# Performance work log

Measured on AMD Instinct MI355X. Metric: run time of the kernel, lower is better.

## Reference

```python
import jax, jax.numpy as jnp
import numpy as np

BETA = 5.0
B, D, K, E2 = 64, 3072, 512, 64


def setup_inputs() -> dict:
    key = jax.random.key(0)
    k1, k2, k3, k4 = jax.random.split(key, 4)
    images = jax.random.normal(k1, (B, D), dtype=jnp.float32)
    w_proj = jax.random.normal(k2, (K, D), dtype=jnp.float32) * 0.02   # project.weight
    w_img2 = jax.random.normal(k3, (K, D * E2), dtype=jnp.float32) * 0.02  # img2.weight
    w_rec = jax.random.normal(k4, (E2, K), dtype=jnp.float32) * 0.02   # rec.weight
    return {"images": images, "w_proj": w_proj, "w_img2": w_img2, "w_rec": w_rec}


def reference(images, w_proj, w_img2, w_rec):
    beta = BETA
    wimg = w_proj.T            # (D, K)
    wrec = w_rec.T             # (K, E2)
    # img2.weight (K, D*E2) -> codebook tensor (K, D, E2), std-normalized over D (ddof=1 to match torch)
    wimg2 = w_img2.reshape(K, D, E2)
    wimg2 = wimg2 / (0.01 + jnp.std(wimg2, axis=1, keepdims=True, ddof=1))

    # ---- encode ----
    xd = images[:, :, None] - wimg[None]          # (B, D, K)
    xh = -jnp.mean(xd * xd, axis=1) * beta        # (B, K)
    xp = jax.nn.softmax(xh, axis=-1)              # (B, K)
    lat1 = xp @ wrec                              # (B, E2)
    xe = jnp.einsum('bdk,kde->bke', xd, wimg2)    # (B, K, E2)
    lat2 = jnp.einsum('bke,bk->be', xe, xp)       # (B, E2)

    # ---- decode ----
    diff = lat1[:, :, None] - wrec.T[None]        # (B, E2, K); wrec.T is (E2, K)
    xh2 = -jnp.mean(diff * diff, axis=1) * beta   # (B, K)
    xp2 = jax.nn.softmax(xh2, axis=-1)            # (B, K)
    xx = xp2[:, :, None] * lat2[:, None, :]       # (B, K, E2)
    xd2 = jnp.einsum('bke,kde->bd', xx, wimg2)    # (B, D)
    images_recon = xp2 @ wimg.T + xd2             # (B, D)

    loss = jnp.mean((images_recon - images) ** 2, axis=-1)  # (B,)
    return loss
```

## Files before the change

kernel.cpp:

```cpp
#include <hip/hip_runtime.h>
#include <math.h>

#define Bn 64
#define Dn 3072
#define Kn 512
#define En 64

static constexpr float BETA = 5.0f;

static constexpr size_t ZF_OFF    = 0;
static constexpr size_t ACCP_OFF  = 1048576;
static constexpr size_t PART_OFF  = 1048576;
static constexpr size_t STATP_OFF = 5242880;
static constexpr size_t S_OFF     = 5439488;
static constexpr size_t PACC_OFF  = 5472256;
static constexpr size_t DOTP_OFF  = 5505024;
static constexpr size_t NPP_OFF   = 5767168;
static constexpr size_t XP2_OFF   = 5771264;
static constexpr size_t XP2B_OFF  = 5804032;
static constexpr size_t LAT2_OFF  = 5820416;
static constexpr size_t WRECT_OFF = 5824512;
static constexpr size_t FRAG_OFF  = 5857280;

typedef float  f4  __attribute__((ext_vector_type(4)));
typedef __bf16 bf8 __attribute__((ext_vector_type(8)));
typedef int    i4  __attribute__((ext_vector_type(4)));

union AB { i4 i; bf8 b; };

__device__ __forceinline__ unsigned short bf16b(float x) {
  __bf16 h = (__bf16)x;
  union Cv { __bf16 h; unsigned short u; } c;
  c.h = h;
  return c.u;
}

__device__ __forceinline__ float waveAllMax(float v) {
#pragma unroll
  for (int o = 32; o; o >>= 1) v = fmaxf(v, __shfl_xor(v, o));
  return v;
}
__device__ __forceinline__ float waveAllSum(float v) {
#pragma unroll
  for (int o = 32; o; o >>= 1) v += __shfl_xor(v, o);
  return v;
}

__global__ __launch_bounds__(256) void kPT(const float* __restrict__ img,
                                           const float* __restrict__ wrec,
                                           float* __restrict__ ws) {
  const int t = threadIdx.x;
  if (blockIdx.x < 96) {
    const int ds = blockIdx.x;
    const int T = t >> 6, l = t & 63;
    const int b = 16 * T + (l & 15);
    const int d0 = 32 * ds + 8 * (l >> 4);
    const float* p = img + (size_t)b * Dn + d0;
    unsigned short u[8];
#pragma unroll
    for (int j = 0; j < 8; ++j) u[j] = bf16b(p[j]);
    i4 v;
    v.x = (int)u[0] | ((int)u[1] << 16);
    v.y = (int)u[2] | ((int)u[3] << 16);
    v.z = (int)u[4] | ((int)u[5] << 16);
    v.w = (int)u[6] | ((int)u[7] << 16);
    ((i4*)(ws + FRAG_OFF))[(ds * 4 + T) * 64 + l] = v;
  } else {
    int g = (blockIdx.x - 96) * 256 + t;
    int k = g >> 6, e = g & 63;
    ws[WRECT_OFF + g] = wrec[(size_t)e * Kn + k];
  }
}

__global__ __launch_bounds__(256) void kDotP(const float* __restrict__ wproj,
                                             float* __restrict__ ws) {
  const int t = threadIdx.x, w = t >> 6, l = t & 63, elane = l & 15, dgrp = l >> 4;
  const int kk = blockIdx.x * 16 + elane;
  const int dc = blockIdx.y;
  const int n0 = dc * 12;
  const i4* afr = (const i4*)(ws + FRAG_OFF);
  const float* wrow = wproj + (size_t)kk * Dn;
  f4 acc = {0.f, 0.f, 0.f, 0.f};
  float np = 0.f;
  float bwA[8], bwB[8];
  i4 avA, avB;
  avA = afr[((size_t)n0 * 4 + w) * 64 + l];
#pragma unroll
  for (int j = 0; j < 8; ++j) bwA[j] = wrow[(size_t)n0 * 32 + 8 * dgrp + j];

#define KD_ITER(BWC, BWN, AVC, AVN, NL) {                                        \
    const int nl1 = (NL) + 1;                                                    \
    if (nl1 < 12) {                                                              \
      AVN = afr[((size_t)(n0 + nl1) * 4 + w) * 64 + l];                          \
      _Pragma("unroll")                                                          \
      for (int j = 0; j < 8; ++j)                                                \
        BWN[j] = wrow[(size_t)(n0 + nl1) * 32 + 8 * dgrp + j];                   \
    }                                                                            \
    bf8 bfr;                                                                     \
    _Pragma("unroll")                                                            \
    for (int j = 0; j < 8; ++j) { float v = BWC[j]; np = fmaf(v, v, np); bfr[j] = (__bf16)v; } \
    AB a; a.i = AVC;                                                             \
    acc = __builtin_amdgcn_mfma_f32_16x16x32_bf16(a.b, bfr, acc, 0, 0, 0);       \
  }

  for (int nl = 0; nl < 12; nl += 2) {
    KD_ITER(bwA, bwB, avA, avB, nl)
    KD_ITER(bwB, bwA, avB, avA, nl + 1)
  }
#undef KD_ITER
#pragma unroll
  for (int r = 0; r < 4; ++r) {
    int b = 16 * w + 4 * dgrp + r;
    ws[DOTP_OFF + (size_t)dc * (Bn * Kn) + (size_t)b * Kn + kk] = acc[r];
  }
  np += __shfl_xor(np, 16);
  np += __shfl_xor(np, 32);
  if (w == 0 && dgrp == 0) ws[NPP_OFF + (size_t)dc * Kn + kk] = np;
}

__global__ __launch_bounds__(256, 4) void kA(const float* __restrict__ wproj,
                                             const float* __restrict__ w2,
                                             float* __restrict__ ws) {
  const int k = blockIdx.x, h = blockIdx.y, t = threadIdx.x;
  const int w = t >> 6, l = t & 63, elane = l & 15, dgrp = l >> 4;
  const int ecol = 16 * w + elane;
  const int n0 = h * 48;
  __shared__ float wp[Dn / 2];
  const float* wpk = wproj + (size_t)k * Dn + (size_t)h * (Dn / 2);
  {
    f4* dst = (f4*)wp;
    const f4* src = (const f4*)wpk;
    dst[t] = src[t];
    if (t < 128) dst[t + 256] = src[t + 256];
  }
  __syncthreads();

  const i4* afr = (const i4*)(ws + FRAG_OFF);
  const float* w2k = w2 + (size_t)k * (Dn * En);
  f4 acc0 = {0.f,0.f,0.f,0.f}, acc1 = {0.f,0.f,0.f,0.f};
  f4 acc2 = {0.f,0.f,0.f,0.f}, acc3 = {0.f,0.f,0.f,0.f};
  float ssum = 0.f, ssq = 0.f, pacc = 0.f;
  float bwA[8], bwB[8];
#pragma unroll
  for (int j = 0; j < 8; ++j)
    bwA[j] = w2k[(size_t)(n0 * 32 + 8 * dgrp + j) * 64 + ecol];

#define KA_ITER(BWC, BWN, NL) {                                                  \
    const int nl1 = (NL) + 1;                                                    \
    if (nl1 < 48) {                                                              \
      _Pragma("unroll")                                                          \
      for (int j = 0; j < 8; ++j)                                                \
        BWN[j] = w2k[(size_t)((n0 + nl1) * 32 + 8 * dgrp + j) * 64 + ecol];      \
    }                                                                            \
    i4 av0 = afr[((size_t)(n0 + (NL)) * 4 + 0) * 64 + l];                        \
    i4 av1 = afr[((size_t)(n0 + (NL)) * 4 + 1) * 64 + l];                        \
    i4 av2 = afr[((size_t)(n0 + (NL)) * 4 + 2) * 64 + l];                        \
    i4 av3 = afr[((size_t)(n0 + (NL)) * 4 + 3) * 64 + l];                        \
    bf8 bfr;                                                                     \
    _Pragma("unroll")                                                            \
    for (int j = 0; j < 8; ++j) {                                                \
      float v = BWC[j];                                                          \
      ssum += v; ssq = fmaf(v, v, ssq);                                          \
      pacc = fmaf(wp[(NL) * 32 + 8 * dgrp + j], v, pacc);                        \
      bfr[j] = (__bf16)v;                                                        \
    }                                                                            \
    AB a0, a1, a2, a3;                                                           \
    a0.i = av0; a1.i = av1; a2.i = av2; a3.i = av3;                              \
    acc0 = __builtin_amdgcn_mfma_f32_16x16x32_bf16(a0.b, bfr, acc0, 0, 0, 0);    \
    acc1 = __builtin_amdgcn_mfma_f32_16x16x32_bf16(a1.b, bfr, acc1, 0, 0, 0);    \
    acc2 = __builtin_amdgcn_mfma_f32_16x16x32_bf16(a2.b, bfr, acc2, 0, 0, 0);    \
    acc3 = __builtin_amdgcn_mfma_f32_16x16x32_bf16(a3.b, bfr, acc3, 0, 0, 0);    \
  }

  for (int nl = 0; nl < 48; nl += 2) {
    KA_ITER(bwA, bwB, nl)
    KA_ITER(bwB, bwA, nl + 1)
  }
#undef KA_ITER

  ssum += __shfl_xor(ssum, 16); ssum += __shfl_xor(ssum, 32);
  ssq  += __shfl_xor(ssq, 16);  ssq  += __shfl_xor(ssq, 32);
  pacc += __shfl_xor(pacc, 16); pacc += __shfl_xor(pacc, 32);
  const size_t kh = (size_t)(k * 2 + h);
  if (dgrp == 0) {
    ws[STATP_OFF + kh * 192 + 0 * 64 + ecol] = ssum;
    ws[STATP_OFF + kh * 192 + 1 * 64 + ecol] = ssq;
    ws[STATP_OFF + kh * 192 + 2 * 64 + ecol] = pacc;
  }
#pragma unroll
  for (int T = 0; T < 4; ++T) {
    f4 a = (T == 0) ? acc0 : (T == 1) ? acc1 : (T == 2) ? acc2 : acc3;
#pragma unroll
    for (int r = 0; r < 4; ++r) {
      int b = 16 * T + 4 * dgrp + r;
      ws[ACCP_OFF + kh * 4096 + (size_t)b * 64 + ecol] = a[r];
    }
  }
}

__global__ __launch_bounds__(64) void kStat(float* __restrict__ ws) {
  const int k = blockIdx.x, e = threadIdx.x;
  const size_t o0 = STATP_OFF + (size_t)(2 * k) * 192;
  const size_t o1 = STATP_OFF + (size_t)(2 * k + 1) * 192;
  float ssum = ws[o0 + e] + ws[o1 + e];
  float ssq  = ws[o0 + 64 + e] + ws[o1 + 64 + e];
  float pacc = ws[o0 + 128 + e] + ws[o1 + 128 + e];
  float var = (ssq - ssum * ssum * (1.0f / Dn)) * (1.0f / (Dn - 1));
  float sv = 1.0f / (0.01f + sqrtf(fmaxf(var, 0.f)));
  ws[S_OFF + (size_t)k * 64 + e] = sv;
  ws[PACC_OFF + (size_t)k * 64 + e] = pacc;
}

__global__ __launch_bounds__(256) void kMid(const float* __restrict__ img,
                                            float* __restrict__ ws) {
  const int b = blockIdx.x;
  const int t = threadIdx.x;
  const int wid = t >> 6, lane = t & 63;
  __shared__ float xp_sh[512];
  __shared__ float red[16];
  __shared__ float scratch[256];
  __shared__ __align__(16) float l1_sh[64];

  float acc = 0.f;
  const f4* irow = (const f4*)(img + (size_t)b * Dn);
#pragma unroll
  for (int i = 0; i < 3; ++i) {
    f4 v = irow[t + 256 * i];
    acc = fmaf(v.x, v.x, acc); acc = fmaf(v.y, v.y, acc);
    acc = fmaf(v.z, v.z, acc); acc = fmaf(v.w, v.w, acc);
  }
  acc = waveAllSum(acc);
  if (lane == 0) red[wid] = acc;
  __syncthreads();
  const float nimg = red[0] + red[1] + red[2] + red[3];

  float d1 = 0.f, d2 = 0.f, npa = 0.f, npb = 0.f;
#pragma unroll
  for (int dc = 0; dc < 8; ++dc) {
    d1  += ws[DOTP_OFF + (size_t)dc * (Bn * Kn) + (size_t)b * Kn + t];
    d2  += ws[DOTP_OFF + (size_t)dc * (Bn * Kn) + (size_t)b * Kn + t + 256];
    npa += ws[NPP_OFF + (size_t)dc * Kn + t];
    npb += ws[NPP_OFF + (size_t)dc * Kn + t + 256];
  }
  const float c = -(BETA / Dn);
  float x1 = c * (nimg - 2.f * d1 + npa);
  float x2 = c * (nimg - 2.f * d2 + npb);

  float m = waveAllMax(fmaxf(x1, x2));
  if (lane == 0) red[4 + wid] = m;
  __syncthreads();
  m = fmaxf(fmaxf(red[4], red[5]), fmaxf(red[6], red[7]));
  float e1 = expf(x1 - m), e2 = expf(x2 - m);
  float sv = waveAllSum(e1 + e2);
  if (lane == 0) red[8 + wid] = sv;
  __syncthreads();
  float inv = 1.f / (red[8] + red[9] + red[10] + red[11]);
  xp_sh[t] = e1 * inv;
  xp_sh[t + 256] = e2 * inv;
  __syncthreads();

  const int e = t & 63, q = t >> 6;
  float lacc = 0.f;
  for (int kk = q * 128; kk < q * 128 + 128; ++kk)
    lacc = fmaf(xp_sh[kk], ws[WRECT_OFF + (size_t)kk * En + e], lacc);
  scratch[q * 64 + e] = lacc;
  __syncthreads();
  if (t < 64)
    l1_sh[t] = scratch[t] + scratch[64 + t] + scratch[128 + t] + scratch[192 + t];
  __syncthreads();

  float l2acc = 0.f;
  for (int kk = q * 128; kk < q * 128 + 128; ++kk) {
    float a = ws[ACCP_OFF + (size_t)(2 * kk) * 4096 + (size_t)b * 64 + e]
            + ws[ACCP_OFF + (size_t)(2 * kk + 1) * 4096 + (size_t)b * 64 + e];
    l2acc = fmaf(xp_sh[kk] * ws[S_OFF + (size_t)kk * 64 + e],
                 a - ws[PACC_OFF + (size_t)kk * 64 + e], l2acc);
  }
  __syncthreads();
  scratch[q * 64 + e] = l2acc;
  __syncthreads();
  if (t < 64)
    ws[LAT2_OFF + (size_t)b * En + t] =
        scratch[t] + scratch[64 + t] + scratch[128 + t] + scratch[192 + t];

  float h1 = 0.f, h2 = 0.f;
#pragma unroll
  for (int i = 0; i < 16; ++i) {
    f4 lv = *(const f4*)&l1_sh[i * 4];
    f4 w1 = *(const f4*)&ws[WRECT_OFF + (size_t)t * En + i * 4];
    f4 w2v = *(const f4*)&ws[WRECT_OFF + ((size_t)t + 256) * En + i * 4];
    float a0 = lv.x - w1.x, a1 = lv.y - w1.y, a2 = lv.z - w1.z, a3 = lv.w - w1.w;
    h1 = fmaf(a0, a0, h1); h1 = fmaf(a1, a1, h1);
    h1 = fmaf(a2, a2, h1); h1 = fmaf(a3, a3, h1);
    float b0 = lv.x - w2v.x, b1 = lv.y - w2v.y, b2 = lv.z - w2v.z, b3 = lv.w - w2v.w;
    h2 = fmaf(b0, b0, h2); h2 = fmaf(b1, b1, h2);
    h2 = fmaf(b2, b2, h2); h2 = fmaf(b3, b3, h2);
  }
  const float c2 = -(BETA / En);
  x1 = c2 * h1; x2 = c2 * h2;

  m = waveAllMax(fmaxf(x1, x2));
  if (lane == 0) red[4 + wid] = m;
  __syncthreads();
  m = fmaxf(fmaxf(red[4], red[5]), fmaxf(red[6], red[7]));
  e1 = expf(x1 - m); e2 = expf(x2 - m);
  sv = waveAllSum(e1 + e2);
  if (lane == 0) red[8 + wid] = sv;
  __syncthreads();
  inv = 1.f / (red[8] + red[9] + red[10] + red[11]);
  float p1 = e1 * inv, p2 = e2 * inv;
  ws[XP2_OFF + (size_t)b * Kn + t] = p1;
  ws[XP2_OFF + (size_t)b * Kn + t + 256] = p2;
  unsigned short* xpb = (unsigned short*)(ws + XP2B_OFF);
  xpb[(size_t)b * Kn + t] = bf16b(p1);
  xpb[(size_t)b * Kn + t + 256] = bf16b(p2);
}

__global__ __launch_bounds__(256) void kZ(float* __restrict__ ws) {
  const int g = blockIdx.x * 256 + threadIdx.x;
  const int S = g >> 8;
  const int T = (g >> 6) & 3;
  const int l = g & 63;
  const int dgrp = l >> 4;
  const int b = 16 * T + (l & 15);
  const int kd0 = S * 32 + 8 * dgrp;
  const int k = kd0 >> 6;
  const int e0 = kd0 & 63;
  const float xp2v = ws[XP2_OFF + (size_t)b * Kn + k];
  unsigned short u[8];
#pragma unroll
  for (int j = 0; j < 8; ++j) {
    float v = xp2v * ws[LAT2_OFF + (size_t)b * En + e0 + j] * ws[S_OFF + (size_t)k * En + e0 + j];
    u[j] = bf16b(v);
  }
  i4 v;
  v.x = (int)u[0] | ((int)u[1] << 16);
  v.y = (int)u[2] | ((int)u[3] << 16);
  v.z = (int)u[4] | ((int)u[5] << 16);
  v.w = (int)u[6] | ((int)u[7] << 16);
  ((i4*)(ws + ZF_OFF))[g] = v;
}

__global__ __launch_bounds__(256, 3) void kB(const float* __restrict__ wproj,
                                             const float* __restrict__ w2,
                                             float* __restrict__ ws) {
  const int dtile = blockIdx.x, ks = blockIdx.y, t = threadIdx.x;
  const int w = t >> 6, l = t & 63, elane = l & 15, dgrp = l >> 4;
  const int d = dtile * 64 + 16 * w + elane;
  const i4* zfr = (const i4*)(ws + ZF_OFF);
  f4 acc0 = {0.f,0.f,0.f,0.f}, acc1 = {0.f,0.f,0.f,0.f};
  f4 acc2 = {0.f,0.f,0.f,0.f}, acc3 = {0.f,0.f,0.f,0.f};
  f4 bwA[2], bwB[2];
  i4 avA[4], avB[4];
  {
    const f4* p = (const f4*)(w2 + ((size_t)(ks * 32) * Dn + d) * En + 8 * dgrp);
    bwA[0] = p[0]; bwA[1] = p[1];
#pragma unroll
    for (int T = 0; T < 4; ++T) avA[T] = zfr[((size_t)(ks * 64) * 4 + T) * 64 + l];
  }

#define KB_ITER(BWC, BWN, AVC, AVN, N) {                                         \
    const int np1 = (N) + 1;                                                     \
    if (np1 < 64) {                                                              \
      const int kk = ks * 32 + (np1 >> 1);                                       \
      const int e0 = (np1 & 1) * 32;                                             \
      const f4* p = (const f4*)(w2 + ((size_t)kk * Dn + d) * En + e0 + 8 * dgrp);\
      BWN[0] = p[0]; BWN[1] = p[1];                                              \
      _Pragma("unroll")                                                          \
      for (int T = 0; T < 4; ++T)                                                \
        AVN[T] = zfr[((size_t)(ks * 64 + np1) * 4 + T) * 64 + l];                \
    }                                                                            \
    bf8 bfr;                                                                     \
    _Pragma("unroll")                                                            \
    for (int j = 0; j < 4; ++j) {                                                \
      bfr[j] = (__bf16)BWC[0][j];                                                \
      bfr[4 + j] = (__bf16)BWC[1][j];                                            \
    }                                                                            \
    AB a0, a1, a2, a3;                                                           \
    a0.i = AVC[0]; a1.i = AVC[1]; a2.i = AVC[2]; a3.i = AVC[3];                  \
    acc0 = __builtin_amdgcn_mfma_f32_16x16x32_bf16(a0.b, bfr, acc0, 0, 0, 0);    \
    acc1 = __builtin_amdgcn_mfma_f32_16x16x32_bf16(a1.b, bfr, acc1, 0, 0, 0);    \
    acc2 = __builtin_amdgcn_mfma_f32_16x16x32_bf16(a2.b, bfr, acc2, 0, 0, 0);    \
    acc3 = __builtin_amdgcn_mfma_f32_16x16x32_bf16(a3.b, bfr, acc3, 0, 0, 0);    \
  }

  for (int n = 0; n < 64; n += 2) {
    KB_ITER(bwA, bwB, avA, avB, n)
    KB_ITER(bwB, bwA, avB, avA, n + 1)
  }
#undef KB_ITER

  {
    const int kk0 = ks * 32;
    bf8 bw;
#pragma unroll
    for (int j = 0; j < 8; ++j)
      bw[j] = (__bf16)wproj[(size_t)(kk0 + 8 * dgrp + j) * Dn + d];
    const unsigned short* xpb = (const unsigned short*)(ws + XP2B_OFF);
    AB a0, a1, a2, a3;
    a0.i = *(const i4*)&xpb[(size_t)(0 * 16 + elane) * Kn + kk0 + 8 * dgrp];
    a1.i = *(const i4*)&xpb[(size_t)(1 * 16 + elane) * Kn + kk0 + 8 * dgrp];
    a2.i = *(const i4*)&xpb[(size_t)(2 * 16 + elane) * Kn + kk0 + 8 * dgrp];
    a3.i = *(const i4*)&xpb[(size_t)(3 * 16 + elane) * Kn + kk0 + 8 * dgrp];
    acc0 = __builtin_amdgcn_mfma_f32_16x16x32_bf16(a0.b, bw, acc0, 0, 0, 0);
    acc1 = __builtin_amdgcn_mfma_f32_16x16x32_bf16(a1.b, bw, acc1, 0, 0, 0);
    acc2 = __builtin_amdgcn_mfma_f32_16x16x32_bf16(a2.b, bw, acc2, 0, 0, 0);
    acc3 = __builtin_amdgcn_mfma_f32_16x16x32_bf16(a3.b, bw, acc3, 0, 0, 0);
  }

#pragma unroll
  for (int T = 0; T < 4; ++T) {
    f4 a = (T == 0) ? acc0 : (T == 1) ? acc1 : (T == 2) ? acc2 : acc3;
#pragma unroll
    for (int r = 0; r < 4; ++r) {
      int b = 16 * T + 4 * dgrp + r;
      ws[PART_OFF + ((size_t)ks * Bn + b) * Dn + d] = a[r];
    }
  }
}

__global__ __launch_bounds__(256) void kLoss(const float* __restrict__ img,
                                             const float* __restrict__ ws,
                                             float* __restrict__ out) {
  const int b = blockIdx.x, t = threadIdx.x;
  __shared__ float red[4];
  float acc = 0.f;
  const f4* p4 = (const f4*)(ws + PART_OFF);
  const f4* i4p = (const f4*)(img + (size_t)b * Dn);
  const int rowq = Dn / 4;
#pragma unroll
  for (int i = 0; i < 3; ++i) {
    int idx = t + 256 * i;
    f4 r = {0.f, 0.f, 0.f, 0.f};
#pragma unroll
    for (int s = 0; s < 16; ++s)
      r += p4[((size_t)s * Bn + b) * rowq + idx];
    f4 v = i4p[idx];
    float dx = r.x - v.x, dy = r.y - v.y, dz = r.z - v.z, dw = r.w - v.w;
    acc = fmaf(dx, dx, acc); acc = fmaf(dy, dy, acc);
    acc = fmaf(dz, dz, acc); acc = fmaf(dw, dw, acc);
  }
  acc = waveAllSum(acc);
  if ((t & 63) == 0) red[t >> 6] = acc;
  __syncthreads();
  if (t == 0) out[b] = (red[0] + red[1] + red[2] + red[3]) * (1.0f / Dn);
}

extern "C" void kernel_launch(void* const* d_in, const int* in_sizes, int n_in,
                              void* d_out, int out_size, void* d_ws, size_t ws_size,
                              hipStream_t stream) {
  const float* img   = (const float*)d_in[0];
  const float* wproj = (const float*)d_in[1];
  const float* w2    = (const float*)d_in[2];
  const float* wrec  = (const float*)d_in[3];
  float* ws  = (float*)d_ws;
  float* out = (float*)d_out;

  hipLaunchKernelGGL(kPT,   dim3(224), dim3(256), 0, stream, img, wrec, ws);
  hipLaunchKernelGGL(kDotP, dim3(32, 8), dim3(256), 0, stream, wproj, ws);
  hipLaunchKernelGGL(kA,    dim3(512, 2), dim3(256), 0, stream, wproj, w2, ws);
  hipLaunchKernelGGL(kStat, dim3(512), dim3(64), 0, stream, ws);
  hipLaunchKernelGGL(kMid,  dim3(64),  dim3(256), 0, stream, img, ws);
  hipLaunchKernelGGL(kZ,    dim3(1024), dim3(256), 0, stream, ws);
  hipLaunchKernelGGL(kB,    dim3(48, 16), dim3(256), 0, stream, wproj, w2, ws);
  hipLaunchKernelGGL(kLoss, dim3(64),  dim3(256), 0, stream, img, ws, out);
}
```

Measured before the change: 254.6 us.

## Fuse image-projection dot products into kA and z-fragment build into kMid

```diff
diff --git a/kernel.cpp b/kernel.cpp
--- a/kernel.cpp
+++ b/kernel.cpp
@@ -15,12 +15,10 @@
 static constexpr size_t S_OFF     = 5439488;
 static constexpr size_t PACC_OFF  = 5472256;
 static constexpr size_t DOTP_OFF  = 5505024;
-static constexpr size_t NPP_OFF   = 5767168;
-static constexpr size_t XP2_OFF   = 5771264;
-static constexpr size_t XP2B_OFF  = 5804032;
-static constexpr size_t LAT2_OFF  = 5820416;
-static constexpr size_t WRECT_OFF = 5824512;
-static constexpr size_t FRAG_OFF  = 5857280;
+static constexpr size_t NPROJ_OFF = 5570560;
+static constexpr size_t XP2B_OFF  = 5571072;
+static constexpr size_t WRECT_OFF = 5587456;
+static constexpr size_t FRAG_OFF  = 5620224;
 
 typedef float  f4  __attribute__((ext_vector_type(4)));
 typedef __bf16 bf8 __attribute__((ext_vector_type(8)));
@@ -72,52 +70,6 @@
   }
 }
 
-__global__ __launch_bounds__(256) void kDotP(const float* __restrict__ wproj,
-                                             float* __restrict__ ws) {
-  const int t = threadIdx.x, w = t >> 6, l = t & 63, elane = l & 15, dgrp = l >> 4;
-  const int kk = blockIdx.x * 16 + elane;
-  const int dc = blockIdx.y;
-  const int n0 = dc * 12;
-  const i4* afr = (const i4*)(ws + FRAG_OFF);
-  const float* wrow = wproj + (size_t)kk * Dn;
-  f4 acc = {0.f, 0.f, 0.f, 0.f};
-  float np = 0.f;
-  float bwA[8], bwB[8];
-  i4 avA, avB;
-  avA = afr[((size_t)n0 * 4 + w) * 64 + l];
-#pragma unroll
-  for (int j = 0; j < 8; ++j) bwA[j] = wrow[(size_t)n0 * 32 + 8 * dgrp + j];
-
-#define KD_ITER(BWC, BWN, AVC, AVN, NL) {                                        \
-    const int nl1 = (NL) + 1;                                                    \
-    if (nl1 < 12) {                                                              \
-      AVN = afr[((size_t)(n0 + nl1) * 4 + w) * 64 + l];                          \
-      _Pragma("unroll")                                                          \
-      for (int j = 0; j < 8; ++j)                                                \
-        BWN[j] = wrow[(size_t)(n0 + nl1) * 32 + 8 * dgrp + j];                   \
-    }                                                                            \
-    bf8 bfr;                                                                     \
-    _Pragma("unroll")                                                            \
-    for (int j = 0; j < 8; ++j) { float v = BWC[j]; np = fmaf(v, v, np); bfr[j] = (__bf16)v; } \
-    AB a; a.i = AVC;                                                             \
-    acc = __builtin_amdgcn_mfma_f32_16x16x32_bf16(a.b, bfr, acc, 0, 0, 0);       \
-  }
-
-  for (int nl = 0; nl < 12; nl += 2) {
-    KD_ITER(bwA, bwB, avA, avB, nl)
-    KD_ITER(bwB, bwA, avB, avA, nl + 1)
-  }
-#undef KD_ITER
-#pragma unroll
-  for (int r = 0; r < 4; ++r) {
-    int b = 16 * w + 4 * dgrp + r;
-    ws[DOTP_OFF + (size_t)dc * (Bn * Kn) + (size_t)b * Kn + kk] = acc[r];
-  }
-  np += __shfl_xor(np, 16);
-  np += __shfl_xor(np, 32);
-  if (w == 0 && dgrp == 0) ws[NPP_OFF + (size_t)dc * Kn + kk] = np;
-}
-
 __global__ __launch_bounds__(256, 4) void kA(const float* __restrict__ wproj,
                                              const float* __restrict__ w2,
                                              float* __restrict__ ws) {
@@ -126,12 +78,19 @@
   const int ecol = 16 * w + elane;
   const int n0 = h * 48;
   __shared__ float wp[Dn / 2];
+  __shared__ __bf16 wpb[Dn / 2];
   const float* wpk = wproj + (size_t)k * Dn + (size_t)h * (Dn / 2);
-  {
-    f4* dst = (f4*)wp;
-    const f4* src = (const f4*)wpk;
-    dst[t] = src[t];
-    if (t < 128) dst[t + 256] = src[t + 256];
+  if (t < 192) {
+    f4 x = ((const f4*)wpk)[2 * t];
+    f4 y = ((const f4*)wpk)[2 * t + 1];
+    ((f4*)wp)[2 * t] = x;
+    ((f4*)wp)[2 * t + 1] = y;
+    i4 v;
+    v.x = (int)bf16b(x.x) | ((int)bf16b(x.y) << 16);
+    v.y = (int)bf16b(x.z) | ((int)bf16b(x.w) << 16);
+    v.z = (int)bf16b(y.x) | ((int)bf16b(y.y) << 16);
+    v.w = (int)bf16b(y.z) | ((int)bf16b(y.w) << 16);
+    ((i4*)wpb)[t] = v;
   }
   __syncthreads();
 
@@ -139,23 +98,27 @@
   const float* w2k = w2 + (size_t)k * (Dn * En);
   f4 acc0 = {0.f,0.f,0.f,0.f}, acc1 = {0.f,0.f,0.f,0.f};
   f4 acc2 = {0.f,0.f,0.f,0.f}, acc3 = {0.f,0.f,0.f,0.f};
+  f4 dac0 = {0.f,0.f,0.f,0.f}, dac1 = {0.f,0.f,0.f,0.f};
+  f4 dac2 = {0.f,0.f,0.f,0.f}, dac3 = {0.f,0.f,0.f,0.f};
   float ssum = 0.f, ssq = 0.f, pacc = 0.f;
   float bwA[8], bwB[8];
+  i4 avA[4], avB[4];
 #pragma unroll
   for (int j = 0; j < 8; ++j)
     bwA[j] = w2k[(size_t)(n0 * 32 + 8 * dgrp + j) * 64 + ecol];
-
-#define KA_ITER(BWC, BWN, NL) {                                                  \
+#pragma unroll
+  for (int T = 0; T < 4; ++T) avA[T] = afr[((size_t)n0 * 4 + T) * 64 + l];
+
+#define KA_STEP(BWC, BWN, AVC, AVN, NL) {                                        \
     const int nl1 = (NL) + 1;                                                    \
     if (nl1 < 48) {                                                              \
       _Pragma("unroll")                                                          \
       for (int j = 0; j < 8; ++j)                                                \
         BWN[j] = w2k[(size_t)((n0 + nl1) * 32 + 8 * dgrp + j) * 64 + ecol];      \
+      _Pragma("unroll")                                                          \
+      for (int T = 0; T < 4; ++T)                                                \
+        AVN[T] = afr[((size_t)(n0 + nl1) * 4 + T) * 64 + l];                     \
     }                                                                            \
-    i4 av0 = afr[((size_t)(n0 + (NL)) * 4 + 0) * 64 + l];                        \
-    i4 av1 = afr[((size_t)(n0 + (NL)) * 4 + 1) * 64 + l];                        \
-    i4 av2 = afr[((size_t)(n0 + (NL)) * 4 + 2) * 64 + l];                        \
-    i4 av3 = afr[((size_t)(n0 + (NL)) * 4 + 3) * 64 + l];                        \
     bf8 bfr;                                                                     \
     _Pragma("unroll")                                                            \
     for (int j = 0; j < 8; ++j) {                                                \
@@ -164,19 +127,24 @@
       pacc = fmaf(wp[(NL) * 32 + 8 * dgrp + j], v, pacc);                        \
       bfr[j] = (__bf16)v;                                                        \
     }                                                                            \
+    bf8 wfr = *(const bf8*)&wpb[(NL) * 32 + 8 * dgrp];                           \
     AB a0, a1, a2, a3;                                                           \
-    a0.i = av0; a1.i = av1; a2.i = av2; a3.i = av3;                              \
+    a0.i = AVC[0]; a1.i = AVC[1]; a2.i = AVC[2]; a3.i = AVC[3];                  \
     acc0 = __builtin_amdgcn_mfma_f32_16x16x32_bf16(a0.b, bfr, acc0, 0, 0, 0);    \
     acc1 = __builtin_amdgcn_mfma_f32_16x16x32_bf16(a1.b, bfr, acc1, 0, 0, 0);    \
     acc2 = __builtin_amdgcn_mfma_f32_16x16x32_bf16(a2.b, bfr, acc2, 0, 0, 0);    \
     acc3 = __builtin_amdgcn_mfma_f32_16x16x32_bf16(a3.b, bfr, acc3, 0, 0, 0);    \
+    dac0 = __builtin_amdgcn_mfma_f32_16x16x32_bf16(a0.b, wfr, dac0, 0, 0, 0);    \
+    dac1 = __builtin_amdgcn_mfma_f32_16x16x32_bf16(a1.b, wfr, dac1, 0, 0, 0);    \
+    dac2 = __builtin_amdgcn_mfma_f32_16x16x32_bf16(a2.b, wfr, dac2, 0, 0, 0);    \
+    dac3 = __builtin_amdgcn_mfma_f32_16x16x32_bf16(a3.b, wfr, dac3, 0, 0, 0);    \
   }
 
   for (int nl = 0; nl < 48; nl += 2) {
-    KA_ITER(bwA, bwB, nl)
-    KA_ITER(bwB, bwA, nl + 1)
-  }
-#undef KA_ITER
+    KA_STEP(bwA, bwB, avA, avB, nl)
+    KA_STEP(bwB, bwA, avB, avA, nl + 1)
+  }
+#undef KA_STEP
 
   ssum += __shfl_xor(ssum, 16); ssum += __shfl_xor(ssum, 32);
   ssq  += __shfl_xor(ssq, 16);  ssq  += __shfl_xor(ssq, 32);
@@ -187,6 +155,17 @@
     ws[STATP_OFF + kh * 192 + 1 * 64 + ecol] = ssq;
     ws[STATP_OFF + kh * 192 + 2 * 64 + ecol] = pacc;
   }
+  if (w == 0 && elane == 0) {
+#pragma unroll
+    for (int T = 0; T < 4; ++T) {
+      f4 d = (T == 0) ? dac0 : (T == 1) ? dac1 : (T == 2) ? dac2 : dac3;
+#pragma unroll
+      for (int r = 0; r < 4; ++r) {
+        int b = 16 * T + 4 * dgrp + r;
+        ws[DOTP_OFF + (size_t)h * (Bn * Kn) + (size_t)b * Kn + k] = d[r];
+      }
+    }
+  }
 #pragma unroll
   for (int T = 0; T < 4; ++T) {
     f4 a = (T == 0) ? acc0 : (T == 1) ? acc1 : (T == 2) ? acc2 : acc3;
@@ -198,7 +177,8 @@
   }
 }
 
-__global__ __launch_bounds__(64) void kStat(float* __restrict__ ws) {
+__global__ __launch_bounds__(64) void kStat(const float* __restrict__ wproj,
+                                            float* __restrict__ ws) {
   const int k = blockIdx.x, e = threadIdx.x;
   const size_t o0 = STATP_OFF + (size_t)(2 * k) * 192;
   const size_t o1 = STATP_OFF + (size_t)(2 * k + 1) * 192;
@@ -209,6 +189,15 @@
   float sv = 1.0f / (0.01f + sqrtf(fmaxf(var, 0.f)));
   ws[S_OFF + (size_t)k * 64 + e] = sv;
   ws[PACC_OFF + (size_t)k * 64 + e] = pacc;
+  float np = 0.f;
+  const float* wr = wproj + (size_t)k * Dn;
+#pragma unroll 8
+  for (int i = 0; i < 48; ++i) {
+    float v = wr[i * 64 + e];
+    np = fmaf(v, v, np);
+  }
+  np = waveAllSum(np);
+  if (e == 0) ws[NPROJ_OFF + k] = np;
 }
 
 __global__ __launch_bounds__(256) void kMid(const float* __restrict__ img,
@@ -218,8 +207,9 @@
   const int wid = t >> 6, lane = t & 63;
   __shared__ float xp_sh[512];
   __shared__ float red[16];
-  __shared__ float scratch[256];
+  __shared__ __align__(16) float scratch[1024];
   __shared__ __align__(16) float l1_sh[64];
+  __shared__ float l2_sh[64];
 
   float acc = 0.f;
   const f4* irow = (const f4*)(img + (size_t)b * Dn);
@@ -234,17 +224,15 @@
   __syncthreads();
   const float nimg = red[0] + red[1] + red[2] + red[3];
 
-  float d1 = 0.f, d2 = 0.f, npa = 0.f, npb = 0.f;
-#pragma unroll
-  for (int dc = 0; dc < 8; ++dc) {
-    d1  += ws[DOTP_OFF + (size_t)dc * (Bn * Kn) + (size_t)b * Kn + t];
-    d2  += ws[DOTP_OFF + (size_t)dc * (Bn * Kn) + (size_t)b * Kn + t + 256];
-    npa += ws[NPP_OFF + (size_t)dc * Kn + t];
-    npb += ws[NPP_OFF + (size_t)dc * Kn + t + 256];
-  }
+  float d1 = ws[DOTP_OFF + (size_t)b * Kn + t]
+           + ws[DOTP_OFF + (size_t)(Bn * Kn) + (size_t)b * Kn + t];
+  float d2 = ws[DOTP_OFF + (size_t)b * Kn + t + 256]
+           + ws[DOTP_OFF + (size_t)(Bn * Kn) + (size_t)b * Kn + t + 256];
+  float np1 = ws[NPROJ_OFF + t];
+  float np2 = ws[NPROJ_OFF + t + 256];
   const float c = -(BETA / Dn);
-  float x1 = c * (nimg - 2.f * d1 + npa);
-  float x2 = c * (nimg - 2.f * d2 + npb);
+  float x1 = c * (nimg - 2.f * d1 + np1);
+  float x2 = c * (nimg - 2.f * d2 + np2);
 
   float m = waveAllMax(fmaxf(x1, x2));
   if (lane == 0) red[4 + wid] = m;
@@ -259,29 +247,47 @@
   xp_sh[t + 256] = e2 * inv;
   __syncthreads();
 
-  const int e = t & 63, q = t >> 6;
-  float lacc = 0.f;
-  for (int kk = q * 128; kk < q * 128 + 128; ++kk)
-    lacc = fmaf(xp_sh[kk], ws[WRECT_OFF + (size_t)kk * En + e], lacc);
-  scratch[q * 64 + e] = lacc;
-  __syncthreads();
-  if (t < 64)
-    l1_sh[t] = scratch[t] + scratch[64 + t] + scratch[128 + t] + scratch[192 + t];
-  __syncthreads();
-
-  float l2acc = 0.f;
-  for (int kk = q * 128; kk < q * 128 + 128; ++kk) {
-    float a = ws[ACCP_OFF + (size_t)(2 * kk) * 4096 + (size_t)b * 64 + e]
-            + ws[ACCP_OFF + (size_t)(2 * kk + 1) * 4096 + (size_t)b * 64 + e];
-    l2acc = fmaf(xp_sh[kk] * ws[S_OFF + (size_t)kk * 64 + e],
-                 a - ws[PACC_OFF + (size_t)kk * 64 + e], l2acc);
-  }
-  __syncthreads();
-  scratch[q * 64 + e] = l2acc;
-  __syncthreads();
-  if (t < 64)
-    ws[LAT2_OFF + (size_t)b * En + t] =
-        scratch[t] + scratch[64 + t] + scratch[128 + t] + scratch[192 + t];
+  const int eq = t & 15, kq = t >> 4;
+  const int k0 = kq * 32;
+  const f4* wrect4 = (const f4*)(ws + WRECT_OFF);
+  f4 l1v = {0.f, 0.f, 0.f, 0.f};
+#pragma unroll 4
+  for (int i = 0; i < 32; ++i) {
+    int k = k0 + i;
+    l1v += xp_sh[k] * wrect4[k * 16 + eq];
+  }
+  ((f4*)scratch)[kq * 16 + eq] = l1v;
+  __syncthreads();
+  if (t < 64) {
+    float s = 0.f;
+#pragma unroll
+    for (int q = 0; q < 16; ++q) s += scratch[q * 64 + t];
+    l1_sh[t] = s;
+  }
+  __syncthreads();
+
+  const f4* accp4 = (const f4*)(ws + ACCP_OFF);
+  const f4* s4 = (const f4*)(ws + S_OFF);
+  const f4* pc4 = (const f4*)(ws + PACC_OFF);
+  f4 l2v = {0.f, 0.f, 0.f, 0.f};
+#pragma unroll 4
+  for (int i = 0; i < 32; ++i) {
+    int k = k0 + i;
+    f4 a0 = accp4[(size_t)(2 * k) * 1024 + b * 16 + eq];
+    f4 a1 = accp4[(size_t)(2 * k + 1) * 1024 + b * 16 + eq];
+    f4 svv = s4[k * 16 + eq];
+    f4 pcc = pc4[k * 16 + eq];
+    l2v += (xp_sh[k] * svv) * ((a0 + a1) - pcc);
+  }
+  __syncthreads();
+  ((f4*)scratch)[kq * 16 + eq] = l2v;
+  __syncthreads();
+  if (t < 64) {
+    float s = 0.f;
+#pragma unroll
+    for (int q = 0; q < 16; ++q) s += scratch[q * 64 + t];
+    l2_sh[t] = s;
+  }
 
   float h1 = 0.f, h2 = 0.f;
 #pragma unroll
@@ -309,36 +315,35 @@
   __syncthreads();
   inv = 1.f / (red[8] + red[9] + red[10] + red[11]);
   float p1 = e1 * inv, p2 = e2 * inv;
-  ws[XP2_OFF + (size_t)b * Kn + t] = p1;
-  ws[XP2_OFF + (size_t)b * Kn + t + 256] = p2;
   unsigned short* xpb = (unsigned short*)(ws + XP2B_OFF);
   xpb[(size_t)b * Kn + t] = bf16b(p1);
   xpb[(size_t)b * Kn + t + 256] = bf16b(p2);
-}
-
-__global__ __launch_bounds__(256) void kZ(float* __restrict__ ws) {
-  const int g = blockIdx.x * 256 + threadIdx.x;
-  const int S = g >> 8;
-  const int T = (g >> 6) & 3;
-  const int l = g & 63;
-  const int dgrp = l >> 4;
-  const int b = 16 * T + (l & 15);
-  const int kd0 = S * 32 + 8 * dgrp;
-  const int k = kd0 >> 6;
-  const int e0 = kd0 & 63;
-  const float xp2v = ws[XP2_OFF + (size_t)b * Kn + k];
-  unsigned short u[8];
-#pragma unroll
-  for (int j = 0; j < 8; ++j) {
-    float v = xp2v * ws[LAT2_OFF + (size_t)b * En + e0 + j] * ws[S_OFF + (size_t)k * En + e0 + j];
-    u[j] = bf16b(v);
-  }
-  i4 v;
-  v.x = (int)u[0] | ((int)u[1] << 16);
-  v.y = (int)u[2] | ((int)u[3] << 16);
-  v.z = (int)u[4] | ((int)u[5] << 16);
-  v.w = (int)u[6] | ((int)u[7] << 16);
-  ((i4*)(ws + ZF_OFF))[g] = v;
+
+  const int T = b >> 4, bl = b & 15;
+  i4* zf = (i4*)(ws + ZF_OFF);
+#pragma unroll
+  for (int kk = 0; kk < 2; ++kk) {
+    const int k = t + 256 * kk;
+    const float p = kk ? p2 : p1;
+#pragma unroll
+    for (int g = 0; g < 8; ++g) {
+      const int dgrp = g & 3;
+      const int S = 2 * k + (g >> 2);
+      const int l = dgrp * 16 + bl;
+      unsigned short u[8];
+#pragma unroll
+      for (int j = 0; j < 8; ++j) {
+        int e = 8 * g + j;
+        u[j] = bf16b(p * l2_sh[e] * ws[S_OFF + (size_t)k * En + e]);
+      }
+      i4 v;
+      v.x = (int)u[0] | ((int)u[1] << 16);
+      v.y = (int)u[2] | ((int)u[3] << 16);
+      v.z = (int)u[4] | ((int)u[5] << 16);
+      v.w = (int)u[6] | ((int)u[7] << 16);
+      zf[((size_t)S * 4 + T) * 64 + l] = v;
+    }
+  }
 }
 
 __global__ __launch_bounds__(256, 3) void kB(const float* __restrict__ wproj,
@@ -457,11 +462,9 @@
   float* out = (float*)d_out;
 
   hipLaunchKernelGGL(kPT,   dim3(224), dim3(256), 0, stream, img, wrec, ws);
-  hipLaunchKernelGGL(kDotP, dim3(32, 8), dim3(256), 0, stream, wproj, ws);
   hipLaunchKernelGGL(kA,    dim3(512, 2), dim3(256), 0, stream, wproj, w2, ws);
-  hipLaunchKernelGGL(kStat, dim3(512), dim3(64), 0, stream, ws);
+  hipLaunchKernelGGL(kStat, dim3(512), dim3(64), 0, stream, wproj, ws);
   hipLaunchKernelGGL(kMid,  dim3(64),  dim3(256), 0, stream, img, ws);
-  hipLaunchKernelGGL(kZ,    dim3(1024), dim3(256), 0, stream, ws);
   hipLaunchKernelGGL(kB,    dim3(48, 16), dim3(256), 0, stream, wproj, w2, ws);
   hipLaunchKernelGGL(kLoss, dim3(64),  dim3(256), 0, stream, img, ws, out);
 }
```

Result: faster. 248.4 us (-2.5%).
